# Kernel tuning notes

Measured on AMD Instinct MI355X. Metric: run time of the kernel, lower is better.

The kernel has to match this reference:

```python
import jax, jax.numpy as jnp
import numpy as np

WSZ = 128                 # window_size from init
TOKEN_SELF = -50000.0     # TOKEN_SELF_ATTN_VALUE
EPS_NORM = 1e-12
EPS_MEAN = 1e-5


def l2norm(x, axis=-1):
    # matches F.normalize(x, 2, dim=-1) with eps=1e-12 (clamp_min on the norm)
    n = jnp.linalg.norm(x, axis=axis, keepdims=True)
    return x / jnp.maximum(n, EPS_NORM)


def shift(x):
    # relative-position shift: [..., i, j] -> [..., i, j] (here i == j == WSZ)
    lead = x.shape[:-2]
    i, j = x.shape[-2], x.shape[-1]
    x = jnp.concatenate([x, jnp.zeros((*lead, i, i), x.dtype)], axis=-1)
    l = i + j - 1
    x = x.reshape(*lead, i * (i + j))
    pad = (-x.shape[-1]) % l
    x = jnp.concatenate([x, jnp.zeros((*lead, pad), x.dtype)], axis=-1)
    x = x.reshape(*lead, -1, l)
    return x[..., :i, i - 1:]


def setup_inputs() -> dict:
    key = jax.random.key(0)
    k1, k2, k3, k4 = jax.random.split(key, 4)
    b, h, t, d, c = 2, 8, 8192, 64, 64
    qk = jax.random.normal(k1, (b, h, t, d), jnp.float32)
    v = jax.random.normal(k2, (b, h, t, d), jnp.float32)
    means = l2norm(jax.random.normal(k3, (h, c, d), jnp.float32))  # EMA kmeans buffer
    rel_weights = jax.random.normal(k4, (WSZ, h, d), jnp.float32) * 0.02
    return {"qk": qk, "v": v, "means": means, "rel_weights": rel_weights}


def reference(qk, v, means, rel_weights):
    b, h, t, d = qk.shape
    wsz = WSZ
    nc = t // wsz
    scale = d ** -0.5

    # ---- routing (torch.no_grad block; eval mode: 0 kmeans iters) ----
    kr = l2norm(qk)                                      # k_routing = F.normalize(qk)
    dists = jnp.einsum('bhtd,hcd->bhtc', kr, means)      # similarity to cluster means
    # topk tokens per cluster (dim=-2 == t), then sort token indices ascending
    topk_idx = jax.lax.top_k(jnp.swapaxes(dists, -1, -2), wsz)[1]  # [b,h,c,wsz]
    indices = jnp.sort(topk_idx, axis=-1)
    idx_flat = indices.reshape(b, h, t)                  # nc*wsz == t

    # ---- gather into clustered windows ----
    qk_g = jnp.take_along_axis(qk, idx_flat[..., None], axis=2)   # [b,h,t,d]
    v_g = jnp.take_along_axis(v, idx_flat[..., None], axis=2)
    q = qk_g.reshape(b, h, nc, wsz, d)
    k = l2norm(qk_g.reshape(b, h, nc, wsz, d))
    v_w = v_g.reshape(b, h, nc, wsz, d)

    # ---- windowed attention with shifted relative position ----
    dots = jnp.einsum('bhnid,bhnjd->bhnij', q, k) * scale
    rel = shift(jnp.einsum('bhnid,jhd->bhnij', q, rel_weights) * scale)
    dots = dots + rel
    eye = jnp.eye(wsz, dtype=bool)
    dots = jnp.where(eye, TOKEN_SELF, dots)              # mask self-attention
    attn = jax.nn.softmax(dots, axis=-1)
    bo = jnp.einsum('bhnij,bhnjd->bhnid', attn, v_w)
    so = bo.reshape(b, h, t, d).astype(jnp.float32)

    # ---- scatter-mean back to original token order ----
    bb = jnp.arange(b)[:, None, None]
    hh = jnp.arange(h)[None, :, None]
    numer = jnp.zeros((b, h, t, d), so.dtype).at[bb, hh, idx_flat].add(so)
    denom = jnp.zeros((b, h, t, d), so.dtype).at[bb, hh, idx_flat].add(jnp.ones_like(so))
    return numer / (denom + EPS_MEAN)
```

## Files before the change

kernel.cpp:

```cpp
#include <hip/hip_runtime.h>
#include <hip/hip_bf16.h>


#define TOKEN_SELF -50000.0f

typedef __attribute__((ext_vector_type(8))) short short8;
typedef __attribute__((ext_vector_type(4))) float f32x4;

__device__ __forceinline__ unsigned short f2bf(float x) {
    union { __hip_bfloat16 b; unsigned short u; } v;
    v.b = __float2bfloat16(x);
    return v.u;
}
__device__ __forceinline__ float bf2f(unsigned short b) {
    return __uint_as_float(((unsigned)b) << 16);
}

__global__ __launch_bounds__(256) void dists_kernel(const float* __restrict__ qk,
                                                    const float* __restrict__ means,
                                                    unsigned* __restrict__ keys) {
    __shared__ float qs[64 * 132];
    __shared__ double ms[64 * 66];
    __shared__ double nrm_part[2][128];
    __shared__ double rden_s[128];
    const int lb = ((blockIdx.x & 7) << 7) + (blockIdx.x >> 3);
    const int tid = threadIdx.x;
    const int bh = lb >> 6;
    const int chunk = lb & 63;
    const int h = bh & 7;
    const int t0 = chunk << 7;

    for (int k = tid; k < 1024; k += 256) {
        float4 f = reinterpret_cast<const float4*>(means + h * 4096)[k];
        const int c = k >> 4, d4 = (k & 15) << 2;
        ms[(d4 + 0) * 66 + c] = (double)f.x;
        ms[(d4 + 1) * 66 + c] = (double)f.y;
        ms[(d4 + 2) * 66 + c] = (double)f.z;
        ms[(d4 + 3) * 66 + c] = (double)f.w;
    }
    {
        const int r = tid & 127, dh = tid >> 7;
        const float4* src = reinterpret_cast<const float4*>(
            qk + (((size_t)bh << 13) + t0 + r) * 64 + dh * 32);
        double n2 = 0.0;
#pragma unroll
        for (int k4 = 0; k4 < 8; ++k4) {
            float4 f = src[k4];
            const int d = dh * 32 + 4 * k4;
            qs[(d + 0) * 132 + r] = f.x;
            qs[(d + 1) * 132 + r] = f.y;
            qs[(d + 2) * 132 + r] = f.z;
            qs[(d + 3) * 132 + r] = f.w;
            n2 += (double)f.x * (double)f.x + (double)f.y * (double)f.y
                + (double)f.z * (double)f.z + (double)f.w * (double)f.w;
        }
        nrm_part[dh][r] = n2;
    }
    __syncthreads();
    if (tid < 128) {
        double den = sqrt(nrm_part[0][tid] + nrm_part[1][tid]);
        rden_s[tid] = 1.0 / (den > 1e-12 ? den : 1e-12);
    }
    __syncthreads();

    const int tok0 = (tid & 31) << 2;
    const int c0 = (tid >> 5) << 3;
    double acc[4][8];
#pragma unroll
    for (int ti = 0; ti < 4; ++ti)
#pragma unroll
        for (int ci = 0; ci < 8; ++ci) acc[ti][ci] = 0.0;

#pragma unroll 2
    for (int d = 0; d < 64; ++d) {
        const float4 qv = *reinterpret_cast<const float4*>(&qs[d * 132 + tok0]);
        const double2 m0 = *reinterpret_cast<const double2*>(&ms[d * 66 + c0 + 0]);
        const double2 m1 = *reinterpret_cast<const double2*>(&ms[d * 66 + c0 + 2]);
        const double2 m2 = *reinterpret_cast<const double2*>(&ms[d * 66 + c0 + 4]);
        const double2 m3 = *reinterpret_cast<const double2*>(&ms[d * 66 + c0 + 6]);
        const double qd[4] = {(double)qv.x, (double)qv.y, (double)qv.z, (double)qv.w};
        const double md[8] = {m0.x, m0.y, m1.x, m1.y, m2.x, m2.y, m3.x, m3.y};
#pragma unroll
        for (int ti = 0; ti < 4; ++ti)
#pragma unroll
            for (int ci = 0; ci < 8; ++ci)
                acc[ti][ci] = fma(qd[ti], md[ci], acc[ti][ci]);
    }

    const double r0 = rden_s[tok0 + 0], r1 = rden_s[tok0 + 1];
    const double r2 = rden_s[tok0 + 2], r3 = rden_s[tok0 + 3];
    unsigned* kb = keys + ((size_t)bh << 19) + t0 + tok0;
#pragma unroll
    for (int ci = 0; ci < 8; ++ci) {
        uint4 wv;
        wv.x = (unsigned)(__double2ll_rn(acc[0][ci] * r0 * 2.0e9) + 2147483648LL);
        wv.y = (unsigned)(__double2ll_rn(acc[1][ci] * r1 * 2.0e9) + 2147483648LL);
        wv.z = (unsigned)(__double2ll_rn(acc[2][ci] * r2 * 2.0e9) + 2147483648LL);
        wv.w = (unsigned)(__double2ll_rn(acc[3][ci] * r3 * 2.0e9) + 2147483648LL);
        *reinterpret_cast<uint4*>(&kb[(size_t)(c0 + ci) << 13]) = wv;
    }
}

__global__ __launch_bounds__(256) void topk_kernel(const unsigned* __restrict__ keys,
                                                   int* __restrict__ idx_out) {
    __shared__ __align__(16) unsigned key[8192];
    __shared__ unsigned cand[1024];
    __shared__ unsigned hist[256];
    __shared__ unsigned s_prefix, s_need, s_cnt, s_nc;
    __shared__ unsigned wg[4], we[4];
    const int lb = ((blockIdx.x & 7) << 7) + (blockIdx.x >> 3);
    const int tid = threadIdx.x;
    const int lane = tid & 63;
    const int w = tid >> 6;

    {
        const uint4* src4 = reinterpret_cast<const uint4*>(keys + ((size_t)lb << 13));
        uint4* k4 = reinterpret_cast<uint4*>(key);
        for (int k = tid; k < 2048; k += 256) k4[k] = src4[k];
    }
    __syncthreads();

    unsigned prefix = 0, need = 128u;
    int ncand = -1;
#pragma unroll
    for (int shift = 24; shift >= 0; shift -= 8) {
        hist[tid] = 0u;
        __syncthreads();
        if (shift == 24) {
            for (int k = tid; k < 8192; k += 256) atomicAdd(&hist[key[k] >> 24], 1u);
        } else {
            const unsigned maskHi = 0xFFFFFFFFu << (shift + 8);
            if (ncand >= 0) {
                for (int k = tid; k < ncand; k += 256) {
                    unsigned u = cand[k];
                    if ((u & maskHi) == prefix) atomicAdd(&hist[(u >> shift) & 255u], 1u);
                }
            } else {
                for (int k = tid; k < 8192; k += 256) {
                    unsigned u = key[k];
                    if ((u & maskHi) == prefix) atomicAdd(&hist[(u >> shift) & 255u], 1u);
                }
            }
        }
        __syncthreads();
        if (tid < 64) {
            unsigned h0 = hist[tid*4], h1 = hist[tid*4+1], h2 = hist[tid*4+2], h3 = hist[tid*4+3];
            unsigned tot = h0 + h1 + h2 + h3;
            unsigned s = tot;
#pragma unroll
            for (int off = 1; off < 64; off <<= 1) {
                unsigned tdown = __shfl_down(s, off);
                if (tid + off < 64) s += tdown;
            }
            const unsigned above = s - tot;
            hist[tid*4+3] = above + h3;
            hist[tid*4+2] = above + h3 + h2;
            hist[tid*4+1] = above + h3 + h2 + h1;
            hist[tid*4+0] = above + tot;
        }
        __syncthreads();
        {
            const unsigned sd = hist[tid];
            const unsigned sd1 = (tid < 255) ? hist[tid + 1] : 0u;
            if (sd >= need && sd1 < need) {
                s_prefix = prefix | ((unsigned)tid << shift);
                s_need = need - sd1;
                s_cnt = sd - sd1;
            }
        }
        __syncthreads();
        prefix = s_prefix;
        need = s_need;
        if (shift == 24) {
            const unsigned cd = s_cnt;
            if (tid == 0) s_nc = 0u;
            __syncthreads();
            if (cd <= 1024u) {
                const unsigned D = prefix >> 24;
                for (int k = tid; k < 8192; k += 256) {
                    unsigned u = key[k];
                    if ((u >> 24) == D) cand[atomicAdd(&s_nc, 1u)] = u;
                }
                ncand = (int)cd;
            }
            __syncthreads();
        }
    }

    const unsigned V = prefix;
    const unsigned rneed = need;
    const int base = tid << 5;
    unsigned cgt = 0, ceq = 0;
#pragma unroll 8
    for (int k = 0; k < 32; ++k) {
        unsigned u = key[base + k];
        cgt += (u > V) ? 1u : 0u;
        ceq += (u == V) ? 1u : 0u;
    }
    unsigned gi = cgt, ei = ceq;
#pragma unroll
    for (int off = 1; off < 64; off <<= 1) {
        unsigned tg = __shfl_up(gi, off);
        unsigned te = __shfl_up(ei, off);
        if (lane >= off) { gi += tg; ei += te; }
    }
    if (lane == 63) { wg[w] = gi; we[w] = ei; }
    __syncthreads();
    unsigned og = 0, oe = 0;
    for (int x = 0; x < w; ++x) { og += wg[x]; oe += we[x]; }
    unsigned g = og + gi - cgt;
    unsigned e = oe + ei - ceq;
    int* out = idx_out + (lb << 7);
    for (int k = 0; k < 32; ++k) {
        unsigned u = key[base + k];
        if (u > V) {
            out[g + (e < rneed ? e : rneed)] = base + k;
            ++g;
        } else if (u == V) {
            if (e < rneed) out[g + e] = base + k;
            ++e;
        }
    }
}

__global__ __launch_bounds__(512, 2) void attn_kernel(const float* __restrict__ qk,
                                                      const float* __restrict__ vv,
                                                      const float* __restrict__ relw,
                                                      const int* __restrict__ idx,
                                                      float* __restrict__ so) {
    __shared__ __align__(16) unsigned short SA[18432];
    __shared__ __align__(16) unsigned short SB[18432];
    __shared__ float invn_s[128];
    __shared__ int idxs_s[128];

    const int lb = ((blockIdx.x & 7) << 7) + (blockIdx.x >> 3);
    const int tid = threadIdx.x;
    const int bh  = lb >> 6;
    const int h   = bh & 7;
    const int wv = tid >> 6, l = tid & 63, g = l >> 4, ln = l & 15;
    const size_t base_bh = ((size_t)bh) << 13;
    const float scale = 0.125f;

    if (tid < 128) idxs_s[tid] = idx[(lb << 7) + tid];
    __syncthreads();

    {
        const int r = tid >> 2, quarter = tid & 3;
        const float4* qsrc = reinterpret_cast<const float4*>(
            qk + (base_bh + idxs_s[r]) * 64 + quarter * 16);
        float x[16]; float nrm = 0.f;
#pragma unroll
        for (int k4 = 0; k4 < 4; ++k4) {
            float4 f = qsrc[k4];
            x[4*k4+0]=f.x; x[4*k4+1]=f.y; x[4*k4+2]=f.z; x[4*k4+3]=f.w;
            nrm += f.x*f.x + f.y*f.y + f.z*f.z + f.w*f.w;
        }
        nrm += __shfl_xor(nrm, 1);
        nrm += __shfl_xor(nrm, 2);
        if (quarter == 0) invn_s[r] = 1.0f / fmaxf(sqrtf(nrm), 1e-12f);
        unsigned short* qhi = SA;
        unsigned short* qlo = SA + 9216;
        const int rb = r * 72 + quarter * 16;
#pragma unroll
        for (int m = 0; m < 8; ++m) {
            unsigned short h0 = f2bf(x[2*m]), h1 = f2bf(x[2*m+1]);
            *(unsigned*)&qhi[rb + 2*m] = (unsigned)h0 | ((unsigned)h1 << 16);
            unsigned short l0 = f2bf(x[2*m] - bf2f(h0));
            unsigned short l1 = f2bf(x[2*m+1] - bf2f(h1));
            *(unsigned*)&qlo[rb + 2*m] = (unsigned)l0 | ((unsigned)l1 << 16);
        }
        float wx[16];
        const float4* wsrc = reinterpret_cast<const float4*>(
            relw + (size_t)(r*8 + h) * 64 + quarter * 16);
#pragma unroll
        for (int k4 = 0; k4 < 4; ++k4) {
            float4 f = wsrc[k4];
            wx[4*k4+0]=f.x; wx[4*k4+1]=f.y; wx[4*k4+2]=f.z; wx[4*k4+3]=f.w;
        }
#pragma unroll
        for (int m = 0; m < 8; ++m) {
            unsigned short w0 = f2bf(wx[2*m]), w1 = f2bf(wx[2*m+1]);
            *(unsigned*)&SB[rb + 2*m] = (unsigned)w0 | ((unsigned)w1 << 16);
        }
    }
    __syncthreads();

    const unsigned short* qhi = SA;
    const unsigned short* qlo = SA + 9216;
    short8 aH[2], aL[2];
#pragma unroll
    for (int kc = 0; kc < 2; ++kc) {
        int ro = (wv*16 + ln) * 72 + kc*32 + g*8;
        aH[kc] = *(const short8*)&qhi[ro];
        aL[kc] = *(const short8*)&qlo[ro];
    }
    f32x4 accD[8], accG[8];
#pragma unroll
    for (int jt = 0; jt < 8; ++jt) {
        accD[jt] = (f32x4)0.f;
        accG[jt] = (f32x4)0.f;
    }
#pragma unroll
    for (int jt = 0; jt < 8; ++jt) {
        const int rb = (jt*16 + ln) * 72 + g*8;
        short8 bH0 = *(const short8*)&qhi[rb];
        short8 bH1 = *(const short8*)&qhi[rb + 32];
        short8 bL0 = *(const short8*)&qlo[rb];
        short8 bL1 = *(const short8*)&qlo[rb + 32];
        short8 w0  = *(const short8*)&SB[rb];
        short8 w1  = *(const short8*)&SB[rb + 32];
        f32x4 d = accD[jt];
        d = __builtin_amdgcn_mfma_f32_16x16x32_bf16(aH[0], bH0, d, 0, 0, 0);
        d = __builtin_amdgcn_mfma_f32_16x16x32_bf16(aH[1], bH1, d, 0, 0, 0);
        d = __builtin_amdgcn_mfma_f32_16x16x32_bf16(aH[0], bL0, d, 0, 0, 0);
        d = __builtin_amdgcn_mfma_f32_16x16x32_bf16(aH[1], bL1, d, 0, 0, 0);
        d = __builtin_amdgcn_mfma_f32_16x16x32_bf16(aL[0], bH0, d, 0, 0, 0);
        d = __builtin_amdgcn_mfma_f32_16x16x32_bf16(aL[1], bH1, d, 0, 0, 0);
        accD[jt] = d;
        f32x4 gg = accG[jt];
        gg = __builtin_amdgcn_mfma_f32_16x16x32_bf16(aH[0], w0, gg, 0, 0, 0);
        gg = __builtin_amdgcn_mfma_f32_16x16x32_bf16(aH[1], w1, gg, 0, 0, 0);
        accG[jt] = gg;
    }
    const int j0 = (tid & 63) * 2, dbase = (tid >> 6) * 8;
    const float4* vs0 = reinterpret_cast<const float4*>(vv + (base_bh + idxs_s[j0])   * 64 + dbase);
    const float4* vs1 = reinterpret_cast<const float4*>(vv + (base_bh + idxs_s[j0+1]) * 64 + dbase);
    float4 va[2], vb[2];
#pragma unroll
    for (int m = 0; m < 2; ++m) { va[m] = vs0[m]; vb[m] = vs1[m]; }
    __syncthreads();

#pragma unroll
    for (int jt = 0; jt < 8; ++jt) {
        const int i0 = wv*16 + g*4;
        const int c = jt*16 + ln;
#pragma unroll
        for (int r = 0; r < 4; ++r)
            SB[(i0 + r)*134 + c] = f2bf(accG[jt][r]);
    }
    {
        unsigned short* vth = SA;
        unsigned short* vtl = SA + 8704;
#pragma unroll
        for (int m = 0; m < 2; ++m) {
            float pa[4] = {va[m].x, va[m].y, va[m].z, va[m].w};
            float pb[4] = {vb[m].x, vb[m].y, vb[m].z, vb[m].w};
#pragma unroll
            for (int e = 0; e < 4; ++e) {
                const int d = dbase + 4*m + e;
                unsigned short h0 = f2bf(pa[e]), h1 = f2bf(pb[e]);
                *(unsigned*)&vth[d*136 + j0] = (unsigned)h0 | ((unsigned)h1 << 16);
                unsigned short l0 = f2bf(pa[e] - bf2f(h0));
                unsigned short l1 = f2bf(pb[e] - bf2f(h1));
                *(unsigned*)&vtl[d*136 + j0] = (unsigned)l0 | ((unsigned)l1 << 16);
            }
        }
    }
    __syncthreads();

    float invc[8];
#pragma unroll
    for (int jt = 0; jt < 8; ++jt) invc[jt] = invn_s[jt*16 + ln];
    float p[8][4];
#pragma unroll
    for (int jt = 0; jt < 8; ++jt) {
        const int c = jt*16 + ln;
#pragma unroll
        for (int r = 0; r < 4; ++r) {
            const int i = wv*16 + g*4 + r;
            float val = accD[jt][r] * (scale * invc[jt]);
            if (c <= i) val += scale * bf2f(SB[i*134 + (127 + c - i)]);
            if (c == i) val = TOKEN_SELF;
            p[jt][r] = val;
        }
    }
#pragma unroll
    for (int r = 0; r < 4; ++r) {
        float m = p[0][r];
#pragma unroll
        for (int jt = 1; jt < 8; ++jt) m = fmaxf(m, p[jt][r]);
        m = fmaxf(m, __shfl_xor(m, 1));
        m = fmaxf(m, __shfl_xor(m, 2));
        m = fmaxf(m, __shfl_xor(m, 4));
        m = fmaxf(m, __shfl_xor(m, 8));
        float s = 0.f;
#pragma unroll
        for (int jt = 0; jt < 8; ++jt) {
            float e = __expf(p[jt][r] - m);
            p[jt][r] = e;
            s += e;
        }
        s += __shfl_xor(s, 1);
        s += __shfl_xor(s, 2);
        s += __shfl_xor(s, 4);
        s += __shfl_xor(s, 8);
        const float rs = 1.0f / s;
#pragma unroll
        for (int jt = 0; jt < 8; ++jt) p[jt][r] *= rs;
    }

    f32x4 accO[4];
#pragma unroll
    for (int nt = 0; nt < 4; ++nt) accO[nt] = (f32x4)0.f;
    unsigned short* phi = SB;
    unsigned short* plo = SB + 9216;
    const unsigned short* vthc = SA;
    const unsigned short* vtlc = SA + 8704;
#pragma unroll
    for (int kh = 0; kh < 2; ++kh) {
        __syncthreads();
#pragma unroll
        for (int jtl = 0; jtl < 4; ++jtl) {
            const int jt = kh*4 + jtl;
#pragma unroll
            for (int r = 0; r < 4; ++r) {
                const int i = wv*16 + g*4 + r;
                const int cs = (jtl*16 + ln) ^ (((i >> 2) & 3) << 3);
                const float pv = p[jt][r];
                const unsigned short hb = f2bf(pv);
                phi[i*72 + cs] = hb;
                plo[i*72 + cs] = f2bf(pv - bf2f(hb));
            }
        }
        __syncthreads();
#pragma unroll
        for (int kc = 0; kc < 2; ++kc) {
            const int i = wv*16 + ln;
            const int jb = (kc*32 + g*8) ^ (((ln >> 2) & 3) << 3);
            short8 aPh = *(const short8*)&phi[i*72 + jb];
            short8 aPl = *(const short8*)&plo[i*72 + jb];
#pragma unroll
            for (int nt = 0; nt < 4; ++nt) {
                const int vo = (nt*16 + ln)*136 + kh*64 + kc*32 + g*8;
                short8 bh_ = *(const short8*)&vthc[vo];
                short8 bl_ = *(const short8*)&vtlc[vo];
                f32x4 o = accO[nt];
                o = __builtin_amdgcn_mfma_f32_16x16x32_bf16(aPh, bh_, o, 0, 0, 0);
                o = __builtin_amdgcn_mfma_f32_16x16x32_bf16(aPh, bl_, o, 0, 0, 0);
                o = __builtin_amdgcn_mfma_f32_16x16x32_bf16(aPl, bh_, o, 0, 0, 0);
                accO[nt] = o;
            }
        }
    }

    float* dst = so + ((size_t)lb << 13);
#pragma unroll
    for (int nt = 0; nt < 4; ++nt)
#pragma unroll
        for (int r = 0; r < 4; ++r) {
            const int i = wv*16 + g*4 + r;
            dst[(i << 6) + nt*16 + ln] = accO[nt][r];
        }
}

__global__ __launch_bounds__(256) void csr_kernel(const int* __restrict__ idx,
                                                  int* __restrict__ perm,
                                                  int* __restrict__ rowstart) {
    __shared__ unsigned bm[16384];
    __shared__ unsigned starts[8192];
    __shared__ unsigned ttmp[256];
    __shared__ unsigned wsum[4];
    const int tid = threadIdx.x;
    const int bh = blockIdx.x;
    const int* ib = idx + (bh << 13);
    for (int k = tid; k < 16384; k += 256) bm[k] = 0u;
    __syncthreads();
    for (int k = tid; k < 8192; k += 256) {
        const int tok = ib[k];
        const int c = k >> 7;
        atomicOr(&bm[(tok << 1) + (c >> 5)], 1u << (c & 31));
    }
    __syncthreads();
    unsigned loc[32];
    unsigned run = 0;
    const int base = tid << 5;
#pragma unroll
    for (int k = 0; k < 32; ++k) {
        loc[k] = run;
        run += __popc(bm[(base + k) << 1]) + __popc(bm[((base + k) << 1) + 1]);
    }
    ttmp[tid] = run;
    __syncthreads();
    const int lane = tid & 63, w = tid >> 6;
    unsigned v = ttmp[tid];
    unsigned inc = v;
#pragma unroll
    for (int off = 1; off < 64; off <<= 1) {
        unsigned t = __shfl_up(inc, off);
        if (lane >= off) inc += t;
    }
    if (lane == 63) wsum[w] = inc;
    __syncthreads();
    unsigned wb = 0;
    for (int x = 0; x < w; ++x) wb += wsum[x];
    const unsigned tbase = wb + inc - v;
    int* rs = rowstart + (bh << 13);
#pragma unroll
    for (int k = 0; k < 32; ++k) {
        const unsigned s = tbase + loc[k];
        rs[base + k] = (int)s;
        starts[base + k] = s;
    }
    __syncthreads();
    int* pm = perm + (bh << 13);
    for (int k = tid; k < 8192; k += 256) {
        const int tok = ib[k];
        const int c = k >> 7;
        const unsigned w0 = bm[tok << 1], w1 = bm[(tok << 1) + 1];
        const unsigned m0 = (c < 32) ? ((1u << c) - 1u) : 0xFFFFFFFFu;
        const unsigned m1 = (c < 32) ? 0u : ((1u << (c - 32)) - 1u);
        const unsigned rank = __popc(w0 & m0) + __popc(w1 & m1);
        pm[starts[tok] + rank] = k;
    }
}

__global__ __launch_bounds__(256) void gather_kernel(const float* __restrict__ so,
                                                     const int* __restrict__ perm,
                                                     const int* __restrict__ rowstart,
                                                     float* __restrict__ out) {
    const int lb = ((blockIdx.x & 7) << 12) + (blockIdx.x >> 3);
    const int wid = (lb << 2) + (threadIdx.x >> 6);
    const int lane = threadIdx.x & 63;
    const int bh = wid >> 13;
    const int tk = wid & 8191;
    const int* rs = rowstart + (bh << 13);
    const int start = rs[tk];
    const int end = (tk == 8191) ? 8192 : rs[tk + 1];
    float acc = 0.f;
    const float* sob = so + ((size_t)bh << 19);
    const int* pmb = perm + (bh << 13);
    for (int e = start; e < end; ++e) {
        const int p = pmb[e];
        acc += sob[((size_t)p << 6) + lane];
    }
    out[((size_t)wid << 6) + lane] = acc / ((float)(end - start) + 1e-5f);
}

extern "C" void kernel_launch(void* const* d_in, const int* in_sizes, int n_in,
                              void* d_out, int out_size, void* d_ws, size_t ws_size,
                              hipStream_t stream) {
    const float* qk    = (const float*)d_in[0];
    const float* vv    = (const float*)d_in[1];
    const float* means = (const float*)d_in[2];
    const float* relw  = (const float*)d_in[3];
    float* out = (float*)d_out;

    char* wsb = (char*)d_ws;
    const size_t keyBytes = (size_t)16 * 64 * 8192 * 4;
    unsigned* keys = (unsigned*)wsb;
    float* so      = (float*)wsb;
    int* idxp      = (int*)(wsb + keyBytes);
    int* permp     = (int*)(wsb + keyBytes + (16 << 15));
    int* rowstartp = (int*)(wsb + keyBytes + 2 * (16 << 15));

    dists_kernel<<<1024, 256, 0, stream>>>(qk, means, keys);
    topk_kernel<<<1024, 256, 0, stream>>>(keys, idxp);
    csr_kernel<<<16, 256, 0, stream>>>(idxp, permp, rowstartp);
    attn_kernel<<<1024, 512, 0, stream>>>(qk, vv, relw, idxp, so);
    gather_kernel<<<32768, 256, 0, stream>>>(so, permp, rowstartp, out);
}
```

Baseline: 150.6 us.

## Replace CSR kernel with atomic per-token position lists built in topk

Removes the 16-block csr_kernel, which built the inverse map with one block per head. The topk kernel now appends each selected position to a per-token fixed-capacity list using a global atomic counter, and the gather kernel reads those counts and lists directly. A memset clears the counters each call. The attention kernel also issues its V gather loads before the MFMA loop to overlap their latency. The change drops a serial low-parallelism stage, at the cost of a 16 MB position-list buffer, scattered atomics, and a nondeterministic summation order in the scatter-mean.

```diff
diff --git a/kernel.cpp b/kernel.cpp
--- a/kernel.cpp
+++ b/kernel.cpp
@@ -102,10 +102,13 @@
 }
 
 __global__ __launch_bounds__(256) void topk_kernel(const unsigned* __restrict__ keys,
-                                                   int* __restrict__ idx_out) {
+                                                   int* __restrict__ idx_out,
+                                                   unsigned short* __restrict__ plist,
+                                                   int* __restrict__ cntp) {
     __shared__ __align__(16) unsigned key[8192];
     __shared__ unsigned cand[1024];
     __shared__ unsigned hist[256];
+    __shared__ int sel[128];
     __shared__ unsigned s_prefix, s_need, s_cnt, s_nc;
     __shared__ unsigned wg[4], we[4];
     const int lb = ((blockIdx.x & 7) << 7) + (blockIdx.x >> 3);
@@ -214,12 +217,22 @@
     for (int k = 0; k < 32; ++k) {
         unsigned u = key[base + k];
         if (u > V) {
-            out[g + (e < rneed ? e : rneed)] = base + k;
+            const unsigned slot = g + (e < rneed ? e : rneed);
+            out[slot] = base + k;
+            sel[slot] = base + k;
             ++g;
         } else if (u == V) {
-            if (e < rneed) out[g + e] = base + k;
+            if (e < rneed) { out[g + e] = base + k; sel[g + e] = base + k; }
             ++e;
         }
+    }
+    __syncthreads();
+    if (tid < 128) {
+        const int bh = lb >> 6;
+        const int tok = sel[tid];
+        const int pos = ((lb & 63) << 7) + tid;
+        const unsigned s = atomicAdd((unsigned*)&cntp[(bh << 13) + tok], 1u);
+        plist[(((size_t)(bh << 13) + tok) << 6) + s] = (unsigned short)pos;
     }
 }
 
@@ -284,6 +297,13 @@
         }
     }
     __syncthreads();
+
+    const int j0 = (tid & 63) * 2, dbase = (tid >> 6) * 8;
+    const float4* vs0 = reinterpret_cast<const float4*>(vv + (base_bh + idxs_s[j0])   * 64 + dbase);
+    const float4* vs1 = reinterpret_cast<const float4*>(vv + (base_bh + idxs_s[j0+1]) * 64 + dbase);
+    float4 va[2], vb[2];
+#pragma unroll
+    for (int m = 0; m < 2; ++m) { va[m] = vs0[m]; vb[m] = vs1[m]; }
 
     const unsigned short* qhi = SA;
     const unsigned short* qlo = SA + 9216;
@@ -322,12 +342,6 @@
         gg = __builtin_amdgcn_mfma_f32_16x16x32_bf16(aH[1], w1, gg, 0, 0, 0);
         accG[jt] = gg;
     }
-    const int j0 = (tid & 63) * 2, dbase = (tid >> 6) * 8;
-    const float4* vs0 = reinterpret_cast<const float4*>(vv + (base_bh + idxs_s[j0])   * 64 + dbase);
-    const float4* vs1 = reinterpret_cast<const float4*>(vv + (base_bh + idxs_s[j0+1]) * 64 + dbase);
-    float4 va[2], vb[2];
-#pragma unroll
-    for (int m = 0; m < 2; ++m) { va[m] = vs0[m]; vb[m] = vs1[m]; }
     __syncthreads();
 
 #pragma unroll
@@ -453,87 +467,24 @@
         }
 }
 
-__global__ __launch_bounds__(256) void csr_kernel(const int* __restrict__ idx,
-                                                  int* __restrict__ perm,
-                                                  int* __restrict__ rowstart) {
-    __shared__ unsigned bm[16384];
-    __shared__ unsigned starts[8192];
-    __shared__ unsigned ttmp[256];
-    __shared__ unsigned wsum[4];
-    const int tid = threadIdx.x;
-    const int bh = blockIdx.x;
-    const int* ib = idx + (bh << 13);
-    for (int k = tid; k < 16384; k += 256) bm[k] = 0u;
-    __syncthreads();
-    for (int k = tid; k < 8192; k += 256) {
-        const int tok = ib[k];
-        const int c = k >> 7;
-        atomicOr(&bm[(tok << 1) + (c >> 5)], 1u << (c & 31));
-    }
-    __syncthreads();
-    unsigned loc[32];
-    unsigned run = 0;
-    const int base = tid << 5;
-#pragma unroll
-    for (int k = 0; k < 32; ++k) {
-        loc[k] = run;
-        run += __popc(bm[(base + k) << 1]) + __popc(bm[((base + k) << 1) + 1]);
-    }
-    ttmp[tid] = run;
-    __syncthreads();
-    const int lane = tid & 63, w = tid >> 6;
-    unsigned v = ttmp[tid];
-    unsigned inc = v;
-#pragma unroll
-    for (int off = 1; off < 64; off <<= 1) {
-        unsigned t = __shfl_up(inc, off);
-        if (lane >= off) inc += t;
-    }
-    if (lane == 63) wsum[w] = inc;
-    __syncthreads();
-    unsigned wb = 0;
-    for (int x = 0; x < w; ++x) wb += wsum[x];
-    const unsigned tbase = wb + inc - v;
-    int* rs = rowstart + (bh << 13);
-#pragma unroll
-    for (int k = 0; k < 32; ++k) {
-        const unsigned s = tbase + loc[k];
-        rs[base + k] = (int)s;
-        starts[base + k] = s;
-    }
-    __syncthreads();
-    int* pm = perm + (bh << 13);
-    for (int k = tid; k < 8192; k += 256) {
-        const int tok = ib[k];
-        const int c = k >> 7;
-        const unsigned w0 = bm[tok << 1], w1 = bm[(tok << 1) + 1];
-        const unsigned m0 = (c < 32) ? ((1u << c) - 1u) : 0xFFFFFFFFu;
-        const unsigned m1 = (c < 32) ? 0u : ((1u << (c - 32)) - 1u);
-        const unsigned rank = __popc(w0 & m0) + __popc(w1 & m1);
-        pm[starts[tok] + rank] = k;
-    }
-}
-
 __global__ __launch_bounds__(256) void gather_kernel(const float* __restrict__ so,
-                                                     const int* __restrict__ perm,
-                                                     const int* __restrict__ rowstart,
+                                                     const unsigned short* __restrict__ plist,
+                                                     const int* __restrict__ cntp,
                                                      float* __restrict__ out) {
     const int lb = ((blockIdx.x & 7) << 12) + (blockIdx.x >> 3);
     const int wid = (lb << 2) + (threadIdx.x >> 6);
     const int lane = threadIdx.x & 63;
     const int bh = wid >> 13;
     const int tk = wid & 8191;
-    const int* rs = rowstart + (bh << 13);
-    const int start = rs[tk];
-    const int end = (tk == 8191) ? 8192 : rs[tk + 1];
+    const int n = cntp[(bh << 13) + tk];
     float acc = 0.f;
     const float* sob = so + ((size_t)bh << 19);
-    const int* pmb = perm + (bh << 13);
-    for (int e = start; e < end; ++e) {
-        const int p = pmb[e];
+    const unsigned short* pl = plist + (((size_t)(bh << 13) + tk) << 6);
+    for (int e = 0; e < n; ++e) {
+        const int p = pl[e];
         acc += sob[((size_t)p << 6) + lane];
     }
-    out[((size_t)wid << 6) + lane] = acc / ((float)(end - start) + 1e-5f);
+    out[((size_t)wid << 6) + lane] = acc / ((float)n + 1e-5f);
 }
 
 extern "C" void kernel_launch(void* const* d_in, const int* in_sizes, int n_in,
@@ -546,16 +497,18 @@
     float* out = (float*)d_out;
 
     char* wsb = (char*)d_ws;
-    const size_t keyBytes = (size_t)16 * 64 * 8192 * 4;
-    unsigned* keys = (unsigned*)wsb;
-    float* so      = (float*)wsb;
-    int* idxp      = (int*)(wsb + keyBytes);
-    int* permp     = (int*)(wsb + keyBytes + (16 << 15));
-    int* rowstartp = (int*)(wsb + keyBytes + 2 * (16 << 15));
-
+    const size_t keyBytes   = (size_t)16 * 64 * 8192 * 4;
+    const size_t idxBytes   = (size_t)16 * 8192 * 4;
+    const size_t plistBytes = (size_t)16 * 8192 * 64 * 2;
+    unsigned* keys        = (unsigned*)wsb;
+    float* so             = (float*)wsb;
+    int* idxp             = (int*)(wsb + keyBytes);
+    unsigned short* plist = (unsigned short*)(wsb + keyBytes + idxBytes);
+    int* cntp             = (int*)(wsb + keyBytes + idxBytes + plistBytes);
+
+    hipMemsetAsync(cntp, 0, (size_t)16 * 8192 * 4, stream);
     dists_kernel<<<1024, 256, 0, stream>>>(qk, means, keys);
-    topk_kernel<<<1024, 256, 0, stream>>>(keys, idxp);
-    csr_kernel<<<16, 256, 0, stream>>>(idxp, permp, rowstartp);
+    topk_kernel<<<1024, 256, 0, stream>>>(keys, idxp, plist, cntp);
     attn_kernel<<<1024, 512, 0, stream>>>(qk, vv, relw, idxp, so);
-    gather_kernel<<<32768, 256, 0, stream>>>(so, permp, rowstartp, out);
-}
+    gather_kernel<<<32768, 256, 0, stream>>>(so, plist, cntp, out);
+}
```

Measured after the change: 136.0 us. 1.11x faster.
